# Optimization experiments

Measured on AMD Instinct MI355X. Metric: run time of the kernel, lower is better.

The kernel has to match this reference:

```python
import jax, jax.numpy as jnp
import numpy as np
from jax import lax

HEADS = 8
L, B, D, H, V, T = 128, 16, 512, 512, 16000, 32


def setup_inputs() -> dict:
    key = jax.random.key(0)
    ks = jax.random.split(key, 16)
    p = lambda k, shape, fan: (jax.random.normal(k, shape, jnp.float32) * (fan ** -0.5))
    output_len = jnp.sort(jax.random.randint(ks[15], (B,), 1, T + 1))[::-1]
    output_len = output_len.at[0].set(T)  # max(output_len) == T, sorted descending
    return dict(
        memory=jax.random.normal(ks[0], (L, B, D), jnp.float32),
        emb=p(ks[1], (V, H), H),
        Wq=p(ks[2], (2 * H, H), 2 * H), bq=jnp.zeros((H,), jnp.float32),
        Wk=p(ks[3], (D, H), D), bk=jnp.zeros((H,), jnp.float32),
        Wv=p(ks[4], (D, H), D), bv=jnp.zeros((H,), jnp.float32),
        W_ih=p(ks[5], (H, 3 * H), H), b_ih=p(ks[6], (3 * H,), H),
        W_hh=p(ks[7], (H, 3 * H), H), b_hh=p(ks[8], (3 * H,), H),
        Wf=p(ks[9], (H, V), H), bf=jnp.zeros((V,), jnp.float32),
        output_len=output_len.astype(jnp.int32),
        max_output_len=T,
    )


def _forward(memory, emb, Wq, bq, Wk, bk, Wv, bv, W_ih, b_ih, W_hh, b_hh, Wf, bf,
             output_len, max_output_len):
    Lm, bs, _ = memory.shape
    Hh = emb.shape[1]
    dk = Hh // HEADS
    scale = 1.0 / np.sqrt(dk)

    def mha(query):  # query: (1, bs, 2H); recomputes k/v projections each step (faithful)
        qh = (query @ Wq + bq).reshape(1, bs, HEADS, dk).transpose(2, 1, 0, 3)   # (h,b,1,dk)
        kh = (memory @ Wk + bk).reshape(Lm, bs, HEADS, dk).transpose(2, 1, 0, 3)  # (h,b,L,dk)
        vh = (memory @ Wv + bv).reshape(Lm, bs, HEADS, dk).transpose(2, 1, 0, 3)
        score = jax.nn.softmax(jnp.einsum('hbqd,hbkd->hbqk', qh, kh) * scale, axis=-1)
        ctx = jnp.einsum('hbqk,hbkd->hbqd', score, vh)          # (h,b,1,dk)
        ctx = ctx.transpose(2, 1, 0, 3).reshape(1, bs, Hh)       # (1,b,H)
        sc = score.transpose(2, 1, 0, 3).mean(axis=2)            # (1,b,L) mean over heads
        return ctx, sc

    def gru_cell(x, h):  # (bs,H),(bs,H) -> (bs,H); PyTorch GRU equations
        gi = x @ W_ih + b_ih
        gh = h @ W_hh + b_hh
        ir, iz, inn = jnp.split(gi, 3, axis=-1)
        hr, hz, hn = jnp.split(gh, 3, axis=-1)
        r = jax.nn.sigmoid(ir + hr)
        z = jax.nn.sigmoid(iz + hz)
        n = jnp.tanh(inn + r * hn)
        return (1.0 - z) * n + z * h

    def step(carry, i):
        out, hid = carry  # (bs,V), (bs,H)
        embedded = emb[jnp.argmax(out, axis=-1)]                 # (bs,H)
        query = jnp.concatenate([embedded, hid], axis=-1)[None]  # (1,bs,2H)
        ctx, sc = mha(query)
        h_new = gru_cell(ctx[0], hid)
        logits = h_new @ Wf + bf                                 # fc on GRU output
        # masking replaces torch's shrinking-batch slicing (output_len sorted desc)
        active = (i < output_len)[:, None].astype(logits.dtype)
        return (logits, h_new), (logits * active, h_new * active, sc[0] * active)

    init = (jnp.zeros((bs, Wf.shape[1]), memory.dtype), jnp.zeros((bs, Hh), memory.dtype))
    _, (outputs, hiddens, scores) = lax.scan(step, init, jnp.arange(max_output_len))
    return outputs, hiddens, scores


def reference(memory, emb, Wq, bq, Wk, bk, Wv, bv, W_ih, b_ih, W_hh, b_hh, Wf, bf,
              output_len, max_output_len):
    return _forward(memory, emb, Wq, bq, Wk, bk, Wv, bv, W_ih, b_ih, W_hh, b_hh,
                    Wf, bf, output_len, max_output_len)
```

## Files before the change

kernel.cpp:

```cpp
#include <hip/hip_runtime.h>

#define LL 128
#define BB 16
#define HH 512
#define VV 16000
#define TT 32
#define NH 8
#define DK 64

#define WS_K 0
#define WS_V (LL*BB*HH)
#define WS_HID0 (2*LL*BB*HH)
#define WS_HID1 (WS_HID0 + BB*HH)
#define WS_CTX  (WS_HID1 + BB*HH)
#define WS_P    (WS_CTX + BB*HH)
#define WS_HS   (WS_P + BB*NH*LL)
#define WS_CAND (WS_HS + BB*HH + 16)
#define WS_WFP  (WS_CAND + 2*512*BB)

#define OUT_HID_OFF ((size_t)TT*BB*VV)
#define OUT_SC_OFF  (OUT_HID_OFF + (size_t)TT*BB*HH)

typedef unsigned long long u64;
__device__ __forceinline__ u64 u64max(u64 a, u64 b) { return a > b ? a : b; }


__global__ __launch_bounds__(256) void kv_kernel(const float* __restrict__ mem,
        const float* __restrict__ Wk, const float* __restrict__ bk,
        const float* __restrict__ Wv, const float* __restrict__ bv,
        const float* __restrict__ Wf, float* __restrict__ ws) {
    int blk = blockIdx.x;
    int tid = threadIdx.x;

    if (blk >= 2048) {
        int m = blk - 2048;
        int colb = m * 32;
        float* dst = ws + WS_WFP + (size_t)m*16384;
        #pragma unroll
        for (int j = 0; j < 16; ++j) {
            int i = tid + 256*j;
            int k = i >> 3, c4 = i & 7;
            float4 v = *(const float4*)(Wf + (size_t)k*VV + colb + c4*4);
            *(float4*)(dst + (size_t)k*32 + c4*4) = v;
        }
        return;
    }

    int rg = blk >> 4, ct = blk & 15;
    int isV = ct >= 8;
    int colbase = (ct & 7) * 64;
    const float* W = isV ? Wv : Wk;
    const float* bias = isV ? bv : bk;
    float* outp = ws + (isV ? WS_V : WS_K);
    int rowbase = rg * 16;
    __shared__ float As[16*516];

    {
        const float4* srcp = (const float4*)(mem + (size_t)rowbase*512);
        #pragma unroll
        for (int j = 0; j < 8; ++j) {
            int i = tid + 256*j;
            float4 v = srcp[i];
            int row = i >> 7, c4i = i & 127;
            *(float4*)(As + row*516 + c4i*4) = v;
        }
    }
    if (blk == 0) {
        for (int i = tid; i < BB*HH; i += 256) ws[WS_HID0 + i] = 0.f;
        u64* cand = (u64*)(ws + WS_CAND);
        for (int i = tid; i < 512*BB; i += 256) cand[i] = 0ull;
    }
    __syncthreads();

    int cq = tid & 15;
    int rq4 = (tid >> 4) & 3;
    int kq = tid >> 6;
    float acc[4][4];
    #pragma unroll
    for (int i = 0; i < 4; ++i) { acc[i][0]=0.f; acc[i][1]=0.f; acc[i][2]=0.f; acc[i][3]=0.f; }
    const float* wp = W + colbase + cq*4;
    for (int k4 = kq*32; k4 < kq*32 + 32; ++k4) {
        float4 a0 = *(const float4*)(As + (rq4*4+0)*516 + k4*4);
        float4 a1 = *(const float4*)(As + (rq4*4+1)*516 + k4*4);
        float4 a2 = *(const float4*)(As + (rq4*4+2)*516 + k4*4);
        float4 a3 = *(const float4*)(As + (rq4*4+3)*516 + k4*4);
        const float* wrow = wp + (size_t)(4*k4)*512;
        float4 w0 = *(const float4*)(wrow);
        float4 w1 = *(const float4*)(wrow + 512);
        float4 w2 = *(const float4*)(wrow + 1024);
        float4 w3 = *(const float4*)(wrow + 1536);
        #define KV_FMA(ri, A) \
            acc[ri][0] += A.x*w0.x + A.y*w1.x + A.z*w2.x + A.w*w3.x; \
            acc[ri][1] += A.x*w0.y + A.y*w1.y + A.z*w2.y + A.w*w3.y; \
            acc[ri][2] += A.x*w0.z + A.y*w1.z + A.z*w2.z + A.w*w3.z; \
            acc[ri][3] += A.x*w0.w + A.y*w1.w + A.z*w2.w + A.w*w3.w;
        KV_FMA(0, a0) KV_FMA(1, a1) KV_FMA(2, a2) KV_FMA(3, a3)
        #undef KV_FMA
    }
    __syncthreads();
    float* red = As;
    #pragma unroll
    for (int ri = 0; ri < 4; ++ri)
        *(float4*)(red + ri*1024 + tid*4) =
            make_float4(acc[ri][0], acc[ri][1], acc[ri][2], acc[ri][3]);
    __syncthreads();
    {
        int c4 = tid & 15, row = tid >> 4;
        int rq = row >> 2, ri = row & 3;
        float4 b4v = *(const float4*)(bias + colbase + c4*4);
        float o[4] = {b4v.x, b4v.y, b4v.z, b4v.w};
        #pragma unroll
        for (int kq2 = 0; kq2 < 4; ++kq2) {
            const float* pr = red + ri*1024 + (kq2*64 + rq*16 + c4)*4;
            o[0] += pr[0]; o[1] += pr[1]; o[2] += pr[2]; o[3] += pr[3];
        }
        *(float4*)(outp + (size_t)(rowbase + row)*512 + colbase + c4*4) =
            make_float4(o[0], o[1], o[2], o[3]);
    }
}

__global__ __launch_bounds__(256) void attn_kernel(
        const float* __restrict__ emb, const float* __restrict__ Wq,
        const float* __restrict__ bq, float* __restrict__ ws, int t) {
    int b = blockIdx.x >> 3, h = blockIdx.x & 7;
    int tid = threadIdx.x;
    const float* hid = ws + ((t & 1) ? WS_HID1 : WS_HID0);
    __shared__ float q[2*HH];
    __shared__ float part[4*64];
    __shared__ float qh[64];
    __shared__ float sp[2*LL];
    __shared__ float p[LL];
    __shared__ float cpart[4*64];
    __shared__ unsigned idx_s;

    if (t > 0) {
        if (tid < 64) {
            const u64* cp = (const u64*)(ws + WS_CAND) + b;
            u64 m = 0ull;
            #pragma unroll
            for (int j = 0; j < 8; ++j)
                m = u64max(m, cp[(size_t)(tid + 64*j)*BB]);
            #pragma unroll
            for (int off = 32; off; off >>= 1)
                m = u64max(m, (u64)__shfl_xor((long long)m, off));
            if (tid == 0) idx_s = 0xFFFFFFFFu - (unsigned)(m & 0xFFFFFFFFull);
        }
    } else if (tid == 0) idx_s = 0u;
    __syncthreads();
    unsigned idx = idx_s;
    for (int i = tid; i < HH; i += 256) {
        q[i] = emb[(size_t)idx*HH + i];
        q[HH + i] = hid[b*HH + i];
    }
    __syncthreads();

    {
        int c4 = tid & 15, kc = tid >> 4;
        const float* wp = Wq + (size_t)kc*HH + h*64 + c4*4;
        float ax=0.f, ay=0.f, az=0.f, aw=0.f;
        #pragma unroll 8
        for (int i = 0; i < 64; ++i) {
            float x = q[kc + 16*i];
            float4 w4 = *(const float4*)wp;
            wp += (size_t)16*HH;
            ax += x*w4.x; ay += x*w4.y; az += x*w4.z; aw += x*w4.w;
        }
        float v;
        v = ax; v += __shfl_xor(v,16); v += __shfl_xor(v,32); ax = v;
        v = ay; v += __shfl_xor(v,16); v += __shfl_xor(v,32); ay = v;
        v = az; v += __shfl_xor(v,16); v += __shfl_xor(v,32); az = v;
        v = aw; v += __shfl_xor(v,16); v += __shfl_xor(v,32); aw = v;
        int wv = tid >> 6;
        if ((tid & 48) == 0)
            *(float4*)(part + wv*64 + c4*4) = make_float4(ax, ay, az, aw);
    }
    __syncthreads();
    if (tid < 64) {
        float s = bq[h*64 + tid];
        #pragma unroll
        for (int wv = 0; wv < 4; ++wv) s += part[wv*64 + tid];
        qh[tid] = s;
    }
    __syncthreads();

    {
        int l = tid & 127, jh = tid >> 7;
        const float4* kr = (const float4*)(ws + WS_K + ((size_t)(l*BB + b))*HH + h*DK) + jh*8;
        const float4* q4 = (const float4*)qh + jh*8;
        float acc = 0.f;
        #pragma unroll
        for (int j = 0; j < 8; ++j) {
            float4 kv = kr[j], qq = q4[j];
            acc += qq.x*kv.x + qq.y*kv.y + qq.z*kv.z + qq.w*kv.w;
        }
        sp[jh*128 + l] = acc;
    }
    __syncthreads();

    if (tid < 64) {
        float s0 = (sp[tid]      + sp[128 + tid]) * 0.125f;
        float s1 = (sp[64 + tid] + sp[192 + tid]) * 0.125f;
        float m = fmaxf(s0, s1);
        #pragma unroll
        for (int off = 32; off; off >>= 1) m = fmaxf(m, __shfl_xor(m, off));
        float e0 = expf(s0 - m), e1 = expf(s1 - m);
        float sum = e0 + e1;
        #pragma unroll
        for (int off = 32; off; off >>= 1) sum += __shfl_xor(sum, off);
        float inv = 1.f / sum;
        p[tid]      = e0 * inv;
        p[64 + tid] = e1 * inv;
    }
    __syncthreads();
    if (tid < 128) ws[WS_P + (size_t)(b*NH + h)*LL + tid] = p[tid];

    {
        int c = tid & 63, lc = tid >> 6;
        const float* Vp = ws + WS_V + h*DK + c;
        float acc = 0.f;
        #pragma unroll 8
        for (int li = 0; li < 32; ++li) {
            int l = lc*32 + li;
            acc += p[l] * Vp[(size_t)(l*BB + b)*HH];
        }
        cpart[lc*64 + c] = acc;
    }
    __syncthreads();
    if (tid < 64)
        ws[WS_CTX + b*HH + h*DK + tid] =
            cpart[tid] + cpart[64+tid] + cpart[128+tid] + cpart[192+tid];
}

__global__ __launch_bounds__(512) void gates_kernel(
        const float* __restrict__ Wih, const float* __restrict__ bih,
        const float* __restrict__ Whh, const float* __restrict__ bhh,
        const int* __restrict__ olen, float* __restrict__ ws,
        float* __restrict__ out, int t) {
    int cb = blockIdx.x;
    int tid = threadIdx.x;
    const float* hid_in = ws + ((t & 1) ? WS_HID1 : WS_HID0);
    float* hid_out = ws + ((t & 1) ? WS_HID0 : WS_HID1);
    const float* ctx = ws + WS_CTX;
    __shared__ float xs[512*20];
    __shared__ float hh[512*20];
    __shared__ float part[3*8*256];
    __shared__ float gacc[6*256];

    for (int i = tid; i < BB*HH; i += 512) {
        int bb = i >> 9, k = i & 511;
        xs[k*20 + bb] = ctx[i];
        hh[k*20 + bb] = hid_in[i];
    }
    if (tid < 64) {
        int e = cb*64 + tid;
        int b = e >> 7, l = e & 127;
        float s = 0.f;
        #pragma unroll
        for (int hq = 0; hq < NH; ++hq)
            s += ws[WS_P + (size_t)(b*NH + hq)*LL + l];
        out[OUT_SC_OFF + ((size_t)t*BB + b)*LL + l] = (t < olen[b]) ? s*0.125f : 0.f;
    }
    __syncthreads();

    int c4 = tid & 3, b4 = (tid >> 2) & 3, kc = tid >> 4;
    int wv = tid >> 6;
    #pragma unroll
    for (int pass = 0; pass < 2; ++pass) {
        const float* W = pass ? Whh : Wih;
        const float* xsrc = pass ? hh : xs;
        float aR[4][4], aZ[4][4], aN[4][4];
        #pragma unroll
        for (int i = 0; i < 4; ++i)
            #pragma unroll
            for (int j = 0; j < 4; ++j) { aR[i][j]=0.f; aZ[i][j]=0.f; aN[i][j]=0.f; }
        const float* wp = W + (size_t)kc*(3*HH) + cb*16 + c4*4;
        const float* xp = xsrc + kc*20 + b4*4;
        #pragma unroll 4
        for (int i = 0; i < 16; ++i) {
            float4 wr = *(const float4*)(wp);
            float4 wz = *(const float4*)(wp + HH);
            float4 wn = *(const float4*)(wp + 2*HH);
            float4 x4 = *(const float4*)xp;
            wp += (size_t)32*(3*HH);
            xp += 32*20;
            #define GR(bi, xv) \
                aR[bi][0] += xv*wr.x; aR[bi][1] += xv*wr.y; aR[bi][2] += xv*wr.z; aR[bi][3] += xv*wr.w; \
                aZ[bi][0] += xv*wz.x; aZ[bi][1] += xv*wz.y; aZ[bi][2] += xv*wz.z; aZ[bi][3] += xv*wz.w; \
                aN[bi][0] += xv*wn.x; aN[bi][1] += xv*wn.y; aN[bi][2] += xv*wn.z; aN[bi][3] += xv*wn.w;
            GR(0, x4.x) GR(1, x4.y) GR(2, x4.z) GR(3, x4.w)
            #undef GR
        }
        #pragma unroll
        for (int bi = 0; bi < 4; ++bi)
            #pragma unroll
            for (int ci = 0; ci < 4; ++ci) {
                float v;
                v = aR[bi][ci]; v += __shfl_xor(v,16); v += __shfl_xor(v,32); aR[bi][ci] = v;
                v = aZ[bi][ci]; v += __shfl_xor(v,16); v += __shfl_xor(v,32); aZ[bi][ci] = v;
                v = aN[bi][ci]; v += __shfl_xor(v,16); v += __shfl_xor(v,32); aN[bi][ci] = v;
            }
        if ((tid & 48) == 0) {
            #pragma unroll
            for (int bi = 0; bi < 4; ++bi) {
                *(float4*)(part + (0*8 + wv)*256 + (b4*4+bi)*16 + c4*4) =
                    make_float4(aR[bi][0], aR[bi][1], aR[bi][2], aR[bi][3]);
                *(float4*)(part + (1*8 + wv)*256 + (b4*4+bi)*16 + c4*4) =
                    make_float4(aZ[bi][0], aZ[bi][1], aZ[bi][2], aZ[bi][3]);
                *(float4*)(part + (2*8 + wv)*256 + (b4*4+bi)*16 + c4*4) =
                    make_float4(aN[bi][0], aN[bi][1], aN[bi][2], aN[bi][3]);
            }
        }
        __syncthreads();
        for (int e2 = tid; e2 < 768; e2 += 512) {
            int g = e2 >> 8, e = e2 & 255;
            float s = 0.f;
            #pragma unroll
            for (int w = 0; w < 8; ++w) s += part[(g*8 + w)*256 + e];
            gacc[(pass*3 + g)*256 + e] = s;
        }
        __syncthreads();
    }

    if (tid < 256) {
        int b = tid >> 4, c = tid & 15;
        int col = cb*16 + c;
        float gir = gacc[0*256 + b*16 + c] + bih[col];
        float giz = gacc[1*256 + b*16 + c] + bih[HH + col];
        float gin = gacc[2*256 + b*16 + c] + bih[2*HH + col];
        float ghr = gacc[3*256 + b*16 + c] + bhh[col];
        float ghz = gacc[4*256 + b*16 + c] + bhh[HH + col];
        float ghn = gacc[5*256 + b*16 + c] + bhh[2*HH + col];
        float r = 1.f/(1.f + __expf(-(gir + ghr)));
        float z = 1.f/(1.f + __expf(-(giz + ghz)));
        float xn = gin + r*ghn;
        float n = 1.f - 2.f/(__expf(2.f*xn) + 1.f);
        float hprev = hh[col*20 + b];
        float hnew = (1.f - z)*n + z*hprev;
        hid_out[b*HH + col] = hnew;
        out[OUT_HID_OFF + ((size_t)t*BB + b)*HH + col] = (t < olen[b]) ? hnew : 0.f;
        ws[WS_HS + col*16 + b] = hnew;
    }
}

__global__ __launch_bounds__(256) void logits_kernel(
        const float* __restrict__ bf, const int* __restrict__ olen,
        float* __restrict__ ws, float* __restrict__ out, int t) {
    __shared__ float hs[HH*20];
    __shared__ float red[4*512];
    __shared__ u64 am[BB*16];
    int tid = threadIdx.x;

    {
        const float4* s4 = (const float4*)(ws + WS_HS);
        #pragma unroll
        for (int j = 0; j < 8; ++j) {
            int i = tid + 256*j;
            float4 v = s4[i];
            int row = i >> 2, qo = i & 3;
            *(float4*)(hs + row*20 + qo*4) = v;
        }
    }
    __syncthreads();

    int c4 = tid & 7, kc = tid >> 3;
    int colbase = blockIdx.x * 32;
    const float* wtile = ws + WS_WFP + (size_t)blockIdx.x*16384;
    float acc[16][4];
    #pragma unroll
    for (int bi = 0; bi < 16; ++bi) { acc[bi][0]=0.f; acc[bi][1]=0.f; acc[bi][2]=0.f; acc[bi][3]=0.f; }
    const float* wp = wtile + (size_t)kc*32 + c4*4;
    const float* hp = hs + kc*20;
    #pragma unroll 8
    for (int i = 0; i < 16; ++i) {
        float4 w4 = *(const float4*)wp;
        float4 h0 = *(const float4*)(hp);
        float4 h1 = *(const float4*)(hp + 4);
        float4 h2 = *(const float4*)(hp + 8);
        float4 h3 = *(const float4*)(hp + 12);
        wp += 32 * 32;
        hp += 32 * 20;
        #define LACC(bi, hv) acc[bi][0] += (hv)*w4.x; acc[bi][1] += (hv)*w4.y; \
                             acc[bi][2] += (hv)*w4.z; acc[bi][3] += (hv)*w4.w;
        LACC(0,h0.x)  LACC(1,h0.y)  LACC(2,h0.z)  LACC(3,h0.w)
        LACC(4,h1.x)  LACC(5,h1.y)  LACC(6,h1.z)  LACC(7,h1.w)
        LACC(8,h2.x)  LACC(9,h2.y)  LACC(10,h2.z) LACC(11,h2.w)
        LACC(12,h3.x) LACC(13,h3.y) LACC(14,h3.z) LACC(15,h3.w)
        #undef LACC
    }

    #pragma unroll
    for (int bi = 0; bi < 16; ++bi)
        #pragma unroll
        for (int ci = 0; ci < 4; ++ci) {
            float v = acc[bi][ci];
            v += __shfl_xor(v, 8);
            v += __shfl_xor(v, 16);
            v += __shfl_xor(v, 32);
            acc[bi][ci] = v;
        }
    int wv = tid >> 6;
    if ((tid & 56) == 0) {
        #pragma unroll
        for (int bi = 0; bi < 16; ++bi)
            *(float4*)(red + wv*512 + bi*32 + c4*4) =
                make_float4(acc[bi][0], acc[bi][1], acc[bi][2], acc[bi][3]);
    }
    __syncthreads();

    {
        int b = tid >> 4, cp = (tid & 15) * 2;
        float2 bf2 = *(const float2*)(bf + colbase + cp);
        float v0 = bf2.x, v1 = bf2.y;
        #pragma unroll
        for (int w = 0; w < 4; ++w) {
            v0 += red[w*512 + b*32 + cp];
            v1 += red[w*512 + b*32 + cp + 1];
        }
        bool active = t < olen[b];
        float2 ov; ov.x = active ? v0 : 0.f; ov.y = active ? v1 : 0.f;
        *(float2*)(out + ((size_t)t*BB + b)*VV + colbase + cp) = ov;

        unsigned u0 = __float_as_uint(v0);
        u0 = (u0 & 0x80000000u) ? ~u0 : (u0 | 0x80000000u);
        unsigned u1 = __float_as_uint(v1);
        u1 = (u1 & 0x80000000u) ? ~u1 : (u1 | 0x80000000u);
        u64 e0 = ((u64)u0 << 32) | (u64)(0xFFFFFFFFu - (unsigned)(colbase + cp));
        u64 e1 = ((u64)u1 << 32) | (u64)(0xFFFFFFFFu - (unsigned)(colbase + cp + 1));
        am[b*16 + (tid & 15)] = e0 > e1 ? e0 : e1;
    }
    __syncthreads();
    if (tid < BB) {
        u64 m = 0ull;
        #pragma unroll
        for (int i = 0; i < 16; ++i) {
            u64 v = am[tid*16 + i];
            m = v > m ? v : m;
        }
        ((u64*)(ws + WS_CAND))[(size_t)blockIdx.x*BB + tid] = m;
    }
}

extern "C" void kernel_launch(void* const* d_in, const int* in_sizes, int n_in,
                              void* d_out, int out_size, void* d_ws, size_t ws_size,
                              hipStream_t stream) {
    const float* mem = (const float*)d_in[0];
    const float* emb = (const float*)d_in[1];
    const float* Wq  = (const float*)d_in[2];
    const float* bq  = (const float*)d_in[3];
    const float* Wk  = (const float*)d_in[4];
    const float* bk  = (const float*)d_in[5];
    const float* Wv  = (const float*)d_in[6];
    const float* bv  = (const float*)d_in[7];
    const float* Wih = (const float*)d_in[8];
    const float* bih = (const float*)d_in[9];
    const float* Whh = (const float*)d_in[10];
    const float* bhh = (const float*)d_in[11];
    const float* Wf  = (const float*)d_in[12];
    const float* bf  = (const float*)d_in[13];
    const int* olen  = (const int*)d_in[14];
    float* out = (float*)d_out;
    float* ws  = (float*)d_ws;

    hipLaunchKernelGGL(kv_kernel, dim3(2548), dim3(256), 0, stream,
                       mem, Wk, bk, Wv, bv, Wf, ws);
    for (int t = 0; t < TT; ++t) {
        hipLaunchKernelGGL(attn_kernel, dim3(BB*NH), dim3(256), 0, stream, emb, Wq, bq, ws, t);
        hipLaunchKernelGGL(gates_kernel, dim3(32), dim3(512), 0, stream,
                           Wih, bih, Whh, bhh, olen, ws, out, t);
        hipLaunchKernelGGL(logits_kernel, dim3(500), dim3(256), 0, stream,
                           bf, olen, ws, out, t);
    }
}
```

Before: 1.250 ms.

## Widen logits tiles to 64 columns with 1024-thread blocks and wave-level argmax

```diff
diff --git a/kernel.cpp b/kernel.cpp
--- a/kernel.cpp
+++ b/kernel.cpp
@@ -34,14 +34,14 @@
 
     if (blk >= 2048) {
         int m = blk - 2048;
-        int colb = m * 32;
-        float* dst = ws + WS_WFP + (size_t)m*16384;
-        #pragma unroll
-        for (int j = 0; j < 16; ++j) {
+        int colb = m * 64;
+        float* dst = ws + WS_WFP + (size_t)m*32768;
+        #pragma unroll
+        for (int j = 0; j < 32; ++j) {
             int i = tid + 256*j;
-            int k = i >> 3, c4 = i & 7;
+            int k = i >> 4, c4 = i & 15;
             float4 v = *(const float4*)(Wf + (size_t)k*VV + colb + c4*4);
-            *(float4*)(dst + (size_t)k*32 + c4*4) = v;
+            *(float4*)(dst + (size_t)k*64 + c4*4) = v;
         }
         return;
     }
@@ -342,19 +342,19 @@
     }
 }
 
-__global__ __launch_bounds__(256) void logits_kernel(
+__global__ __launch_bounds__(1024) void logits_kernel(
         const float* __restrict__ bf, const int* __restrict__ olen,
         float* __restrict__ ws, float* __restrict__ out, int t) {
     __shared__ float hs[HH*20];
-    __shared__ float red[4*512];
-    __shared__ u64 am[BB*16];
+    __shared__ float red[16*1024];
     int tid = threadIdx.x;
+    int lane = tid & 63, wv = tid >> 6;
 
     {
         const float4* s4 = (const float4*)(ws + WS_HS);
         #pragma unroll
-        for (int j = 0; j < 8; ++j) {
-            int i = tid + 256*j;
+        for (int j = 0; j < 2; ++j) {
+            int i = tid + 1024*j;
             float4 v = s4[i];
             int row = i >> 2, qo = i & 3;
             *(float4*)(hs + row*20 + qo*4) = v;
@@ -362,30 +362,38 @@
     }
     __syncthreads();
 
-    int c4 = tid & 7, kc = tid >> 3;
-    int colbase = blockIdx.x * 32;
-    const float* wtile = ws + WS_WFP + (size_t)blockIdx.x*16384;
+    int cq = lane & 15;
+    int kc = wv*4 + (lane >> 4);
+    int colbase = blockIdx.x * 64;
+    const float* wtile = ws + WS_WFP + (size_t)blockIdx.x*32768;
+
     float acc[16][4];
     #pragma unroll
     for (int bi = 0; bi < 16; ++bi) { acc[bi][0]=0.f; acc[bi][1]=0.f; acc[bi][2]=0.f; acc[bi][3]=0.f; }
-    const float* wp = wtile + (size_t)kc*32 + c4*4;
-    const float* hp = hs + kc*20;
-    #pragma unroll 8
-    for (int i = 0; i < 16; ++i) {
-        float4 w4 = *(const float4*)wp;
-        float4 h0 = *(const float4*)(hp);
-        float4 h1 = *(const float4*)(hp + 4);
-        float4 h2 = *(const float4*)(hp + 8);
-        float4 h3 = *(const float4*)(hp + 12);
-        wp += 32 * 32;
-        hp += 32 * 20;
-        #define LACC(bi, hv) acc[bi][0] += (hv)*w4.x; acc[bi][1] += (hv)*w4.y; \
-                             acc[bi][2] += (hv)*w4.z; acc[bi][3] += (hv)*w4.w;
-        LACC(0,h0.x)  LACC(1,h0.y)  LACC(2,h0.z)  LACC(3,h0.w)
-        LACC(4,h1.x)  LACC(5,h1.y)  LACC(6,h1.z)  LACC(7,h1.w)
-        LACC(8,h2.x)  LACC(9,h2.y)  LACC(10,h2.z) LACC(11,h2.w)
-        LACC(12,h3.x) LACC(13,h3.y) LACC(14,h3.z) LACC(15,h3.w)
-        #undef LACC
+
+    #pragma unroll
+    for (int half = 0; half < 2; ++half) {
+        float4 wr[4];
+        const float* wp = wtile + (size_t)(kc + 256*half)*64 + cq*4;
+        #pragma unroll
+        for (int i = 0; i < 4; ++i) { wr[i] = *(const float4*)wp; wp += 4096; }
+        #pragma unroll
+        for (int i = 0; i < 4; ++i) {
+            int k = kc + 256*half + 64*i;
+            float4 w4 = wr[i];
+            const float* hp = hs + k*20;
+            float4 h0 = *(const float4*)(hp);
+            float4 h1 = *(const float4*)(hp + 4);
+            float4 h2 = *(const float4*)(hp + 8);
+            float4 h3 = *(const float4*)(hp + 12);
+            #define LACC(bi, hv) acc[bi][0] += (hv)*w4.x; acc[bi][1] += (hv)*w4.y; \
+                                 acc[bi][2] += (hv)*w4.z; acc[bi][3] += (hv)*w4.w;
+            LACC(0,h0.x)  LACC(1,h0.y)  LACC(2,h0.z)  LACC(3,h0.w)
+            LACC(4,h1.x)  LACC(5,h1.y)  LACC(6,h1.z)  LACC(7,h1.w)
+            LACC(8,h2.x)  LACC(9,h2.y)  LACC(10,h2.z) LACC(11,h2.w)
+            LACC(12,h3.x) LACC(13,h3.y) LACC(14,h3.z) LACC(15,h3.w)
+            #undef LACC
+        }
     }
 
     #pragma unroll
@@ -393,50 +401,34 @@
         #pragma unroll
         for (int ci = 0; ci < 4; ++ci) {
             float v = acc[bi][ci];
-            v += __shfl_xor(v, 8);
             v += __shfl_xor(v, 16);
             v += __shfl_xor(v, 32);
             acc[bi][ci] = v;
         }
-    int wv = tid >> 6;
-    if ((tid & 56) == 0) {
+    if ((lane & 48) == 0) {
         #pragma unroll
         for (int bi = 0; bi < 16; ++bi)
-            *(float4*)(red + wv*512 + bi*32 + c4*4) =
+            *(float4*)(red + wv*1024 + bi*64 + cq*4) =
                 make_float4(acc[bi][0], acc[bi][1], acc[bi][2], acc[bi][3]);
     }
     __syncthreads();
 
     {
-        int b = tid >> 4, cp = (tid & 15) * 2;
-        float2 bf2 = *(const float2*)(bf + colbase + cp);
-        float v0 = bf2.x, v1 = bf2.y;
-        #pragma unroll
-        for (int w = 0; w < 4; ++w) {
-            v0 += red[w*512 + b*32 + cp];
-            v1 += red[w*512 + b*32 + cp + 1];
-        }
+        int b = wv, col = lane;
+        float v = bf[colbase + col];
+        #pragma unroll
+        for (int w = 0; w < 16; ++w) v += red[w*1024 + b*64 + col];
         bool active = t < olen[b];
-        float2 ov; ov.x = active ? v0 : 0.f; ov.y = active ? v1 : 0.f;
-        *(float2*)(out + ((size_t)t*BB + b)*VV + colbase + cp) = ov;
-
-        unsigned u0 = __float_as_uint(v0);
-        u0 = (u0 & 0x80000000u) ? ~u0 : (u0 | 0x80000000u);
-        unsigned u1 = __float_as_uint(v1);
-        u1 = (u1 & 0x80000000u) ? ~u1 : (u1 | 0x80000000u);
-        u64 e0 = ((u64)u0 << 32) | (u64)(0xFFFFFFFFu - (unsigned)(colbase + cp));
-        u64 e1 = ((u64)u1 << 32) | (u64)(0xFFFFFFFFu - (unsigned)(colbase + cp + 1));
-        am[b*16 + (tid & 15)] = e0 > e1 ? e0 : e1;
-    }
-    __syncthreads();
-    if (tid < BB) {
-        u64 m = 0ull;
-        #pragma unroll
-        for (int i = 0; i < 16; ++i) {
-            u64 v = am[tid*16 + i];
-            m = v > m ? v : m;
-        }
-        ((u64*)(ws + WS_CAND))[(size_t)blockIdx.x*BB + tid] = m;
+        __builtin_nontemporal_store(active ? v : 0.f,
+            out + ((size_t)t*BB + b)*VV + colbase + col);
+        unsigned u = __float_as_uint(v);
+        u = (u & 0x80000000u) ? ~u : (u | 0x80000000u);
+        u64 e = ((u64)u << 32) | (u64)(0xFFFFFFFFu - (unsigned)(colbase + col));
+        #pragma unroll
+        for (int off = 32; off; off >>= 1)
+            e = u64max(e, (u64)__shfl_xor((long long)e, off));
+        if (lane == 0)
+            ((u64*)(ws + WS_CAND))[(size_t)blockIdx.x*BB + b] = e;
     }
 }
 
@@ -461,13 +453,13 @@
     float* out = (float*)d_out;
     float* ws  = (float*)d_ws;
 
-    hipLaunchKernelGGL(kv_kernel, dim3(2548), dim3(256), 0, stream,
+    hipLaunchKernelGGL(kv_kernel, dim3(2298), dim3(256), 0, stream,
                        mem, Wk, bk, Wv, bv, Wf, ws);
     for (int t = 0; t < TT; ++t) {
         hipLaunchKernelGGL(attn_kernel, dim3(BB*NH), dim3(256), 0, stream, emb, Wq, bq, ws, t);
         hipLaunchKernelGGL(gates_kernel, dim3(32), dim3(512), 0, stream,
                            Wih, bih, Whh, bhh, olen, ws, out, t);
-        hipLaunchKernelGGL(logits_kernel, dim3(500), dim3(256), 0, stream,
+        hipLaunchKernelGGL(logits_kernel, dim3(250), dim3(1024), 0, stream,
                            bf, olen, ws, out, t);
     }
 }
```

After: 1.403 ms. 1.12x slower.
